# Kernel optimization log

Hardware: AMD Instinct MI355X
Metric: run time of the kernel (lower is better)

## Reference

```python
import jax, jax.numpy as jnp
import numpy as np

NUM_HEADS = 8
SPLIT_S = 4
DIM = 288            # n_feat * 3 * 3
SCALE = (DIM // NUM_HEADS) ** -0.5  # quirk: uses full dim's head_dim (36), not reduced
EPS = 1e-5


def _extract_patches(x):
    # x: [B,C,H,W] -> [B, C*9, H*W], 3x3 kernel, stride 1, 'same' padding
    B, C, H, W = x.shape
    xp = jnp.pad(x, ((0, 0), (0, 0), (1, 1), (1, 1)))
    pats = jnp.stack([xp[:, :, i:i + H, j:j + W] for i in range(3) for j in range(3)], axis=2)
    return pats.reshape(B, C * 9, H * W)


def _fold(cols, H, W):
    # inverse of extract: [B, C*9, H*W] -> [B,C,H,W], summing overlapping patches
    B, Ck, _ = cols.shape
    C = Ck // 9
    p = cols.reshape(B, C, 3, 3, H, W)
    out = jnp.zeros((B, C, H + 2, W + 2), cols.dtype)
    for i in range(3):
        for j in range(3):
            out = out.at[:, :, i:i + H, j:j + W].add(p[:, :, i, j])
    return out[:, :, 1:H + 1, 1:W + 1]


def _ln(x, w, b):
    mu = x.mean(-1, keepdims=True)
    var = ((x - mu) ** 2).mean(-1, keepdims=True)
    return (x - mu) * jax.lax.rsqrt(var + EPS) * w + b


def _attn(x, reduce_w, qkv_w, proj_w, proj_b):
    # x: [B,N,288] -> reduce -> [B,N,144] -> block-diag attention over s=4 chunks
    x = x @ reduce_w.T
    B, N, C = x.shape
    hd = C // NUM_HEADS
    qkv = (x @ qkv_w.T).reshape(B, N, 3, NUM_HEADS, hd).transpose(2, 0, 3, 1, 4)
    q, k, v = qkv[0], qkv[1], qkv[2]          # [B,h,N,hd]
    chunk = N // SPLIT_S
    q = q.reshape(B, NUM_HEADS, SPLIT_S, chunk, hd)
    k = k.reshape(B, NUM_HEADS, SPLIT_S, chunk, hd)
    v = v.reshape(B, NUM_HEADS, SPLIT_S, chunk, hd)
    attn = jnp.einsum('bhscd,bhsed->bhsce', q, k) * SCALE   # [B,h,s,chunk,chunk]
    attn = jax.nn.softmax(attn, axis=-1)
    out = jnp.einsum('bhsce,bhsed->bhscd', attn, v)          # [B,h,s,chunk,hd]
    out = out.transpose(0, 2, 3, 1, 4).reshape(B, N, C)      # cat chunks on token dim
    return out @ proj_w.T + proj_b


def setup_inputs() -> dict:
    key = jax.random.key(0)
    ks = jax.random.split(key, 12)
    d, dr, dh = DIM, DIM // 2, DIM // 4  # 288, 144, 72
    f = lambda k, shape: (jax.random.normal(k, shape, jnp.float32) * 0.02)
    return {
        'x': jax.random.normal(ks[0], (4, 32, 64, 64), jnp.float32),
        'ln1_w': jnp.ones((d,), jnp.float32), 'ln1_b': jnp.zeros((d,), jnp.float32),
        'reduce_w': f(ks[1], (dr, d)),
        'qkv_w': f(ks[2], (3 * dr, dr)),
        'proj_w': f(ks[3], (d, dr)), 'proj_b': jnp.zeros((d,), jnp.float32),
        'ln2_w': jnp.ones((d,), jnp.float32), 'ln2_b': jnp.zeros((d,), jnp.float32),
        'fc1_w': f(ks[4], (dh, d)), 'fc1_b': jnp.zeros((dh,), jnp.float32),
        'fc2_w': f(ks[5], (d, dh)), 'fc2_b': jnp.zeros((d,), jnp.float32),
    }


def reference(x, ln1_w, ln1_b, reduce_w, qkv_w, proj_w, proj_b, ln2_w, ln2_b, fc1_w, fc1_b, fc2_w, fc2_b):
    B, C, H, W = x.shape
    t = _extract_patches(x).transpose(0, 2, 1)  # [B, N=H*W, 288]
    t = t + _attn(_ln(t, ln1_w, ln1_b), reduce_w, qkv_w, proj_w, proj_b)
    h = _ln(t, ln2_w, ln2_b)
    t = t + (jax.nn.relu(h @ fc1_w.T + fc1_b) @ fc2_w.T + fc2_b)
    return _fold(t.transpose(0, 2, 1), H, W)
```

## Files before the change

### kernel.cpp

```cpp
#include <hip/hip_runtime.h>
#include <hip/hip_bf16.h>

typedef __hip_bfloat16 bf16;
typedef unsigned short u16;
typedef unsigned int u32;
typedef __attribute__((ext_vector_type(8))) short bf16x8;
typedef __attribute__((ext_vector_type(4))) float f32x4;

#define BB 4
#define CCH 32
#define HH 64
#define WW 64
#define NN 4096
#define D 288
#define DR 144
#define DQ 432
#define NH 8
#define HD 18
#define SPLIT 4
#define CHUNK 1024
#define KS 512
#define DH 72
#define SCALE_ 0.16666666666666666f
#define QSCALE 0.24044917348149343f
#define EPS_ 1e-5f
#define ASTR 160
#define ATS 168
#define HSTR 96

__device__ __attribute__((aligned(16))) u16 g_Wcb[DQ * D];
__device__ __attribute__((aligned(16))) u16 g_pw[D * ASTR];
__device__ __attribute__((aligned(16))) u16 g_f1w[HSTR * D];
__device__ __attribute__((aligned(16))) u16 g_f2w[D * HSTR];
__device__ __attribute__((aligned(16))) u16 g_q[(size_t)BB * NH * NN * 32];
__device__ __attribute__((aligned(16))) u16 g_k[(size_t)BB * NH * NN * 32];
__device__ __attribute__((aligned(16))) u16 g_vt[(size_t)BB * NH * SPLIT * 32 * CHUNK];
__device__ __attribute__((aligned(16))) float g_part[2 * (size_t)BB * NH * NN * 20];
__device__ __attribute__((aligned(16))) u16 g_h[(size_t)BB * NN * HSTR];
__device__ __attribute__((aligned(16))) u16 g_t0[(size_t)BB * NN * D];
__device__ __attribute__((aligned(16))) u16 g_t1[(size_t)BB * NN * D];
__device__ __attribute__((aligned(16))) u16 g_t2b[(size_t)BB * D * NN];
__device__ int   g_flag;

__device__ __forceinline__ float b2f(bf16 v) { return __bfloat162float(v); }
__device__ __forceinline__ float bits2f(u16 u) { return __uint_as_float(((u32)u) << 16); }
__device__ __forceinline__ u16 f2bits(float f) {
    u32 u = __float_as_uint(f);
    return (u16)((u + 0x7FFF + ((u >> 16) & 1)) >> 16);
}
__device__ __forceinline__ float ldin(const void* p, size_t i, int isbf) {
    return isbf ? b2f(((const bf16*)p)[i]) : ((const float*)p)[i];
}

#define RS  (D * ASTR + HSTR * D + D * HSTR)
#define RS2 (RS + BB * NH * SPLIT * CHUNK)
#define RSB ((RS2 + 255) / 256)
#define PATCHB (BB * HH)

__global__ void k_prep(const void* __restrict__ x, const void* __restrict__ qkv_w,
                       const void* __restrict__ reduce_w, const void* __restrict__ proj_w,
                       const void* __restrict__ fc1_w, const void* __restrict__ fc2_w) {
    __shared__ int cnt4[4];
    __shared__ float qw[DR];
    __shared__ float slab[32 * 3 * 66];
    int tid = threadIdx.x;
    {
        const u16* u = (const u16*)x;
        int c = 0;
        for (int i = tid; i < 2048; i += 256) c += (((u[i] >> 7) & 0xFF) >= 0x90);
        for (int o = 32; o; o >>= 1) c += __shfl_xor(c, o);
        if ((tid & 63) == 0) cnt4[tid >> 6] = c;
    }
    __syncthreads();
    int bf = (cnt4[0] + cnt4[1] + cnt4[2] + cnt4[3]) < 32;
    if (tid == 0 && blockIdx.x == 0) g_flag = bf;

    int bid = blockIdx.x;
    if (bid < DQ) {
        int o = bid;
        if (tid < DR) qw[tid] = ldin(qkv_w, (size_t)o * DR + tid, bf);
        __syncthreads();
        for (int col = tid; col < D; col += 256) {
            float s0 = 0.f, s1 = 0.f;
            #pragma unroll 4
            for (int j = 0; j < DR; j += 2) {
                s0 += qw[j] * ldin(reduce_w, (size_t)j * D + col, bf);
                s1 += qw[j + 1] * ldin(reduce_w, (size_t)(j + 1) * D + col, bf);
            }
            g_Wcb[(size_t)o * D + col] = f2bits(s0 + s1);
        }
    } else if (bid < DQ + RSB) {
        int idx = (bid - DQ) * 256 + tid;
        if (idx < D * ASTR) {
            int o = idx / ASTR, j = idx % ASTR;
            g_pw[idx] = (j < DR) ? f2bits(ldin(proj_w, (size_t)o * DR + j, bf)) : (u16)0;
        } else if (idx < D * ASTR + HSTR * D) {
            int t = idx - D * ASTR;
            int o = t / D;
            g_f1w[t] = (o < DH) ? f2bits(ldin(fc1_w, (size_t)t, bf)) : (u16)0;
        } else if (idx < RS) {
            int t = idx - D * ASTR - HSTR * D;
            int o = t / HSTR, j = t % HSTR;
            g_f2w[t] = (j < DH) ? f2bits(ldin(fc2_w, (size_t)o * DH + j, bf)) : (u16)0;
        } else if (idx < RS2) {
            int t = idx - RS;
            int bhs = t >> 10, n = t & 1023;
            g_vt[((size_t)bhs * 32 + 18) * CHUNK + n] = 0x3F80;
        }
    } else {
        int pb = bid - DQ - RSB;
        int b = pb >> 6, y = pb & 63;
        for (int idx = tid; idx < 32 * 3 * 66; idx += 256) {
            int c = idx / 198, rem = idx % 198;
            int ki = rem / 66, col = rem % 66 - 1;
            int sy = y + ki - 1;
            float v = 0.f;
            if (col >= 0 && col < 64 && sy >= 0 && sy < 64)
                v = ldin(x, ((size_t)(b * CCH + c) * HH + sy) * WW + col, bf);
            slab[idx] = v;
        }
        __syncthreads();
        size_t obase = ((size_t)b * NN + y * 64) * D;
        for (int idx = tid; idx < 64 * D; idx += 256) {
            int t = idx / D, f = idx % D;
            int c = f / 9, k = f % 9, ki = k / 3, kj = k % 3;
            g_t0[obase + idx] = f2bits(slab[c * 198 + ki * 66 + t + kj]);
        }
    }
}

__global__ void k_ln_qkv(const void* __restrict__ lnw, const void* __restrict__ lnb) {
    __shared__ __attribute__((aligned(16))) u16 xln[16 * 296];
    __shared__ float lnwf[D], lnbf[D];
    __shared__ float smu[16], srs[16];
    __shared__ u16 buf[3][144][16];
    int bf = g_flag;
    int tid = threadIdx.x;
    size_t tok0 = (size_t)blockIdx.x * 16;
    for (int i = tid; i < D; i += 256) { lnwf[i] = ldin(lnw, i, bf); lnbf[i] = ldin(lnb, i, bf); }
    {
        int tt = tid >> 4, p = tid & 15;
        const u32* pr = (const u32*)(g_t0 + (tok0 + tt) * D + p * 18);
        float s = 0.f, q = 0.f;
        #pragma unroll
        for (int j = 0; j < 9; ++j) {
            u32 v = pr[j];
            float a = bits2f((u16)(v & 0xFFFF)), b = bits2f((u16)(v >> 16));
            s += a + b; q += a * a + b * b;
        }
        #pragma unroll
        for (int o = 1; o < 16; o <<= 1) { s += __shfl_xor(s, o); q += __shfl_xor(q, o); }
        if (p == 0) {
            float mu = s / D;
            smu[tt] = mu;
            srs[tt] = rsqrtf(q / D - mu * mu + EPS_);
        }
    }
    __syncthreads();
    for (int idx = tid; idx < 16 * 144; idx += 256) {
        int t = idx / 144, dw = idx % 144;
        u32 v = *(const u32*)(g_t0 + (tok0 + t) * D + 2 * dw);
        float mu = smu[t], rs = srs[t];
        int f = 2 * dw;
        float a = (bits2f((u16)(v & 0xFFFF)) - mu) * rs * lnwf[f] + lnbf[f];
        float b = (bits2f((u16)(v >> 16)) - mu) * rs * lnwf[f + 1] + lnbf[f + 1];
        *(u32*)&xln[t * 296 + f] = (u32)f2bits(a) | ((u32)f2bits(b) << 16);
    }
    __syncthreads();
    int w = tid >> 6, lane = tid & 63, quad = lane >> 4, l15 = lane & 15;
    bf16x8 areg[9];
    const u16* abase = xln + l15 * 296 + quad * 8;
    #pragma unroll
    for (int ks = 0; ks < 9; ++ks) areg[ks] = *(const bf16x8*)(abase + ks * 32);
    int nt0 = w * 7, nt1 = (nt0 + 7 > 27) ? 27 : nt0 + 7;
    for (int nt = nt0; nt < nt1; ++nt) {
        f32x4 acc = {0.f, 0.f, 0.f, 0.f};
        const u16* bbase = g_Wcb + (size_t)(nt * 16 + l15) * D + quad * 8;
        #pragma unroll
        for (int ks = 0; ks < 9; ++ks) {
            bf16x8 bfr = *(const bf16x8*)(bbase + ks * 32);
            acc = __builtin_amdgcn_mfma_f32_16x16x32_bf16(areg[ks], bfr, acc, 0, 0, 0);
        }
        int o = nt * 16 + l15;
        int which = o / DR, rem = o % DR;
        #pragma unroll
        for (int r = 0; r < 4; ++r)
            buf[which][rem][quad * 4 + r] = f2bits(which == 0 ? acc[r] * QSCALE : acc[r]);
    }
    __syncthreads();
    {
        int b_ = (int)(tok0 >> 12);
        int n0 = (int)(tok0 & 4095);
        int sIdx = n0 >> 10, nc = n0 & 1023;
        for (int idx = tid; idx < 2 * 8 * 16 * 9; idx += 256) {
            int which = idx / 1152;
            int r2 = idx - which * 1152;
            int h = r2 / 144, r3 = r2 % 144, t = r3 / 9, dw = r3 % 9;
            u32 lo = buf[which][h * 18 + 2 * dw][t];
            u32 hi = buf[which][h * 18 + 2 * dw + 1][t];
            u16* dst = (which ? g_k : g_q) + ((size_t)(b_ * NH + h) * NN + n0 + t) * 32 + 2 * dw;
            *(u32*)dst = lo | (hi << 16);
        }
        for (int idx = tid; idx < 144 * 8; idx += 256) {
            int rem = idx >> 3, tp = idx & 7;
            int hh = rem / HD, dd = rem % HD;
            u32 lo = buf[2][rem][2 * tp];
            u32 hi = buf[2][rem][2 * tp + 1];
            size_t voff = (((size_t)(b_ * NH + hh) * SPLIT + sIdx) * 32 + dd) * CHUNK + nc + 2 * tp;
            *(u32*)&g_vt[voff] = lo | (hi << 16);
        }
    }
}

#define PSTR 72
__global__ __launch_bounds__(128) void k_attn() {
    __shared__ __attribute__((aligned(16))) u16 Pl[2][4][16 * PSTR];
    int bid = blockIdx.x;
    int chunk = bid & 127;
    int qblk = (bid >> 7) & 7;
    int ksl = bid >> 10;
    int s = chunk & 3, bh = chunk >> 2;
    int tid = threadIdx.x;
    int w = tid >> 6, lane = tid & 63, quad = lane >> 4, l15 = lane & 15;

    size_t rowbase = (size_t)bh * NN + s * CHUNK;
    size_t vtbase = ((size_t)bh * SPLIT + s) * 32 * CHUNK;
    const u16* kbase = g_k + rowbase * 32 + quad * 8;
    const u16* vbase = g_vt + vtbase + quad * 8;

    int qbase = qblk * 128 + w * 64;
    bf16x8 qf[4];
    #pragma unroll
    for (int t = 0; t < 4; ++t)
        qf[t] = *(const bf16x8*)(g_q + (rowbase + qbase + t * 16 + l15) * 32 + quad * 8);

    f32x4 accA[4], accB[4];
    #pragma unroll
    for (int t = 0; t < 4; ++t) {
        accA[t] = (f32x4){0.f, 0.f, 0.f, 0.f};
        accB[t] = (f32x4){0.f, 0.f, 0.f, 0.f};
    }

    int kt0 = ksl * KS;
    for (int kk = 0; kk < KS; kk += 64) {
        int kt = kt0 + kk;
        bf16x8 kf0 = *(const bf16x8*)(kbase + (size_t)(kt + 2 * l15) * 32);
        bf16x8 kf1 = *(const bf16x8*)(kbase + (size_t)(kt + 2 * l15 + 1) * 32);
        bf16x8 kf2 = *(const bf16x8*)(kbase + (size_t)(kt + 32 + 2 * l15) * 32);
        bf16x8 kf3 = *(const bf16x8*)(kbase + (size_t)(kt + 33 + 2 * l15) * 32);
        bf16x8 vA0 = *(const bf16x8*)(vbase + (size_t)l15 * CHUNK + kt);
        bf16x8 vB0 = *(const bf16x8*)(vbase + (size_t)(16 + l15) * CHUNK + kt);
        bf16x8 vA1 = *(const bf16x8*)(vbase + (size_t)l15 * CHUNK + kt + 32);
        bf16x8 vB1 = *(const bf16x8*)(vbase + (size_t)(16 + l15) * CHUNK + kt + 32);
        f32x4 z = {0.f, 0.f, 0.f, 0.f};
        #pragma unroll
        for (int t = 0; t < 4; ++t) {
            u16* pw = Pl[w][t];
            f32x4 S0 = __builtin_amdgcn_mfma_f32_16x16x32_bf16(qf[t], kf0, z, 0, 0, 0);
            f32x4 S1 = __builtin_amdgcn_mfma_f32_16x16x32_bf16(qf[t], kf1, z, 0, 0, 0);
            f32x4 S2 = __builtin_amdgcn_mfma_f32_16x16x32_bf16(qf[t], kf2, z, 0, 0, 0);
            f32x4 S3 = __builtin_amdgcn_mfma_f32_16x16x32_bf16(qf[t], kf3, z, 0, 0, 0);
            #pragma unroll
            for (int r = 0; r < 4; ++r) {
                float p0 = exp2f(S0[r]), p1 = exp2f(S1[r]);
                float p2 = exp2f(S2[r]), p3 = exp2f(S3[r]);
                u32 w0 = __builtin_amdgcn_perm(__float_as_uint(p1), __float_as_uint(p0), 0x07060302u);
                u32 w1 = __builtin_amdgcn_perm(__float_as_uint(p3), __float_as_uint(p2), 0x07060302u);
                *(u32*)&pw[(quad * 4 + r) * PSTR + 2 * l15] = w0;
                *(u32*)&pw[(quad * 4 + r) * PSTR + 32 + 2 * l15] = w1;
            }
        }
        #pragma unroll
        for (int t = 0; t < 4; ++t) {
            const u16* pw = Pl[w][t];
            bf16x8 pf0 = *(const bf16x8*)&pw[l15 * PSTR + quad * 8];
            bf16x8 pf1 = *(const bf16x8*)&pw[l15 * PSTR + 32 + quad * 8];
            accA[t] = __builtin_amdgcn_mfma_f32_16x16x32_bf16(pf0, vA0, accA[t], 0, 0, 0);
            accB[t] = __builtin_amdgcn_mfma_f32_16x16x32_bf16(pf0, vB0, accB[t], 0, 0, 0);
            accA[t] = __builtin_amdgcn_mfma_f32_16x16x32_bf16(pf1, vA1, accA[t], 0, 0, 0);
            accB[t] = __builtin_amdgcn_mfma_f32_16x16x32_bf16(pf1, vB1, accB[t], 0, 0, 0);
        }
    }
    float* pb = g_part + (((size_t)ksl * 32 + bh) * SPLIT + s) * (size_t)(CHUNK * 20);
    #pragma unroll
    for (int t = 0; t < 4; ++t) {
        #pragma unroll
        for (int r = 0; r < 4; ++r) {
            int tokenc = qbase + t * 16 + quad * 4 + r;
            float* row = pb + (size_t)tokenc * 20;
            row[l15] = accA[t][r];
            if (l15 < 3) row[16 + l15] = accB[t][r];
        }
    }
}

__global__ void k_proj_ln_fc1(const void* __restrict__ proj_b, const void* __restrict__ lnw,
                              const void* __restrict__ lnb, const void* __restrict__ fc1_b) {
    __shared__ float t1f[16][290];
    __shared__ __attribute__((aligned(16))) u16 xln[16 * 296];
    __shared__ __attribute__((aligned(16))) u16 attnT[16 * ATS];
    __shared__ float lnwf[D], lnbf[D];
    __shared__ float smu[16], srs[16];
    int bf = g_flag;
    int tid = threadIdx.x;
    size_t tok0 = (size_t)blockIdx.x * 16;
    int w = tid >> 6, lane = tid & 63, quad = lane >> 4, l15 = lane & 15;
    for (int i = tid; i < D; i += 256) { lnwf[i] = ldin(lnw, i, bf); lnbf[i] = ldin(lnb, i, bf); }

    int b_ = (int)(tok0 >> 12);
    int s_ = ((int)tok0 & 4095) >> 10;
    int tc0 = (int)tok0 & 1023;
    for (int idx = tid; idx < 16 * (ATS - DR); idx += 256) {
        int t = idx / (ATS - DR), f = idx % (ATS - DR);
        attnT[t * ATS + DR + f] = 0;
    }
    if (tid < 128) {
        int t = tid >> 3, h = tid & 7;
        const float* p1 = g_part + (((size_t)(b_ * NH + h)) * SPLIT + s_) * (size_t)(CHUNK * 20)
                        + (size_t)(tc0 + t) * 20;
        const float* p2 = p1 + (size_t)32 * SPLIT * CHUNK * 20;
        f32x4 a0 = *(const f32x4*)p1,        c0 = *(const f32x4*)p2;
        f32x4 a1 = *(const f32x4*)(p1 + 4),  c1 = *(const f32x4*)(p2 + 4);
        f32x4 a2 = *(const f32x4*)(p1 + 8),  c2 = *(const f32x4*)(p2 + 8);
        f32x4 a3 = *(const f32x4*)(p1 + 12), c3 = *(const f32x4*)(p2 + 12);
        f32x4 a4 = *(const f32x4*)(p1 + 16), c4 = *(const f32x4*)(p2 + 16);
        float inv = 1.f / (a4[2] + c4[2]);
        u16* dst = attnT + t * ATS + h * HD;
        #pragma unroll
        for (int d = 0; d < 4; ++d) {
            dst[d]      = f2bits((a0[d] + c0[d]) * inv);
            dst[4 + d]  = f2bits((a1[d] + c1[d]) * inv);
            dst[8 + d]  = f2bits((a2[d] + c2[d]) * inv);
            dst[12 + d] = f2bits((a3[d] + c3[d]) * inv);
        }
        dst[16] = f2bits((a4[0] + c4[0]) * inv);
        dst[17] = f2bits((a4[1] + c4[1]) * inv);
    }
    __syncthreads();

    {
        bf16x8 areg[5];
        const u16* abase = attnT + l15 * ATS + quad * 8;
        #pragma unroll
        for (int ks = 0; ks < 5; ++ks) areg[ks] = *(const bf16x8*)(abase + ks * 32);
        const int tab[5] = {0, 5, 10, 14, 18};
        for (int nt = tab[w]; nt < tab[w + 1]; ++nt) {
            f32x4 acc = {0.f, 0.f, 0.f, 0.f};
            const u16* bbase = g_pw + (size_t)(nt * 16 + l15) * ASTR + quad * 8;
            #pragma unroll
            for (int ks = 0; ks < 5; ++ks) {
                bf16x8 bfr = *(const bf16x8*)(bbase + ks * 32);
                acc = __builtin_amdgcn_mfma_f32_16x16x32_bf16(areg[ks], bfr, acc, 0, 0, 0);
            }
            int o = nt * 16 + l15;
            float bias = ldin(proj_b, o, bf);
            #pragma unroll
            for (int r = 0; r < 4; ++r) {
                size_t token = tok0 + quad * 4 + r;
                size_t off = token * D + o;
                float val = bits2f(g_t0[off]) + acc[r] + bias;
                g_t1[off] = f2bits(val);
                t1f[quad * 4 + r][o] = val;
            }
        }
    }
    __syncthreads();
    {
        int tt = tid >> 4, p = tid & 15;
        const float* src = &t1f[tt][p * 18];
        float s = 0.f, q = 0.f;
        #pragma unroll
        for (int j = 0; j < 18; ++j) { float a = src[j]; s += a; q += a * a; }
        #pragma unroll
        for (int o = 1; o < 16; o <<= 1) { s += __shfl_xor(s, o); q += __shfl_xor(q, o); }
        if (p == 0) {
            float mu = s / D;
            smu[tt] = mu;
            srs[tt] = rsqrtf(q / D - mu * mu + EPS_);
        }
    }
    __syncthreads();
    for (int idx = tid; idx < 16 * 144; idx += 256) {
        int t = idx / 144, dw = idx % 144;
        int f = 2 * dw;
        float mu = smu[t], rs = srs[t];
        float a = (t1f[t][f] - mu) * rs * lnwf[f] + lnbf[f];
        float b = (t1f[t][f + 1] - mu) * rs * lnwf[f + 1] + lnbf[f + 1];
        *(u32*)&xln[t * 296 + f] = (u32)f2bits(a) | ((u32)f2bits(b) << 16);
    }
    __syncthreads();
    {
        bf16x8 areg[9];
        const u16* abase = xln + l15 * 296 + quad * 8;
        #pragma unroll
        for (int ks = 0; ks < 9; ++ks) areg[ks] = *(const bf16x8*)(abase + ks * 32);
        const int tab2[5] = {0, 2, 4, 5, 6};
        for (int nt = tab2[w]; nt < tab2[w + 1]; ++nt) {
            f32x4 acc = {0.f, 0.f, 0.f, 0.f};
            const u16* bbase = g_f1w + (size_t)(nt * 16 + l15) * D + quad * 8;
            #pragma unroll
            for (int ks = 0; ks < 9; ++ks) {
                bf16x8 bfr = *(const bf16x8*)(bbase + ks * 32);
                acc = __builtin_amdgcn_mfma_f32_16x16x32_bf16(areg[ks], bfr, acc, 0, 0, 0);
            }
            int o = nt * 16 + l15;
            float bias = (o < DH) ? ldin(fc1_b, o, bf) : 0.f;
            #pragma unroll
            for (int r = 0; r < 4; ++r) {
                size_t token = tok0 + quad * 4 + r;
                g_h[token * HSTR + o] = f2bits(fmaxf(acc[r] + bias, 0.f));
            }
        }
    }
}

__global__ void k_fc2(const void* __restrict__ fc2_b) {
    __shared__ float t2f[16][293];
    int bf = g_flag;
    int tid = threadIdx.x;
    size_t tok0 = (size_t)blockIdx.x * 16;
    int w = tid >> 6, lane = tid & 63, quad = lane >> 4, l15 = lane & 15;
    bf16x8 areg[3];
    const u16* abase = g_h + (tok0 + l15) * HSTR + quad * 8;
    #pragma unroll
    for (int ks = 0; ks < 3; ++ks) areg[ks] = *(const bf16x8*)(abase + ks * 32);
    const int tab[5] = {0, 5, 10, 14, 18};
    for (int nt = tab[w]; nt < tab[w + 1]; ++nt) {
        f32x4 acc = {0.f, 0.f, 0.f, 0.f};
        const u16* bbase = g_f2w + (size_t)(nt * 16 + l15) * HSTR + quad * 8;
        #pragma unroll
        for (int ks = 0; ks < 3; ++ks) {
            bf16x8 bfr = *(const bf16x8*)(bbase + ks * 32);
            acc = __builtin_amdgcn_mfma_f32_16x16x32_bf16(areg[ks], bfr, acc, 0, 0, 0);
        }
        int o = nt * 16 + l15;
        float bias = ldin(fc2_b, o, bf);
        #pragma unroll
        for (int r = 0; r < 4; ++r) {
            size_t token = tok0 + quad * 4 + r;
            t2f[quad * 4 + r][o] = bits2f(g_t1[token * D + o]) + acc[r] + bias;
        }
    }
    __syncthreads();
    int b_ = (int)(tok0 >> 12), n0 = (int)(tok0 & 4095);
    for (int idx = tid; idx < D * 8; idx += 256) {
        int o = idx >> 3, tp = idx & 7;
        u32 v = (u32)f2bits(t2f[2 * tp][o]) | ((u32)f2bits(t2f[2 * tp + 1][o]) << 16);
        *(u32*)&g_t2b[((size_t)b_ * D + o) * NN + n0 + 2 * tp] = v;
    }
}

__global__ void k_fold(void* __restrict__ out) {
    int bf = g_flag;
    int idx = blockIdx.x * blockDim.x + threadIdx.x;
    if (idx >= BB * CCH * HH * WW) return;
    int xx = idx % WW;
    int y = (idx / WW) % HH;
    int c = (idx / (WW * HH)) % CCH;
    int b = idx / (WW * HH * CCH);
    const u16* base = g_t2b + ((size_t)b * D + c * 9) * NN;
    float s = 0.f;
    #pragma unroll
    for (int i = 0; i < 3; ++i) {
        int sy = y + 1 - i;
        if (sy < 0 || sy >= HH) continue;
        #pragma unroll
        for (int j = 0; j < 3; ++j) {
            int sx = xx + 1 - j;
            if (sx < 0 || sx >= WW) continue;
            s += bits2f(base[(size_t)(i * 3 + j) * NN + sy * WW + sx]);
        }
    }
    if (bf) ((bf16*)out)[idx] = __float2bfloat16(s);
    else    ((float*)out)[idx] = s;
}

extern "C" void kernel_launch(void* const* d_in, const int* in_sizes, int n_in,
                              void* d_out, int out_size, void* d_ws, size_t ws_size,
                              hipStream_t stream) {
    const void* x        = d_in[0];
    const void* ln1_w    = d_in[1];
    const void* ln1_b    = d_in[2];
    const void* reduce_w = d_in[3];
    const void* qkv_w    = d_in[4];
    const void* proj_w   = d_in[5];
    const void* proj_b   = d_in[6];
    const void* ln2_w    = d_in[7];
    const void* ln2_b    = d_in[8];
    const void* fc1_w    = d_in[9];
    const void* fc1_b    = d_in[10];
    const void* fc2_w    = d_in[11];
    const void* fc2_b    = d_in[12];

    k_prep        <<<DQ + RSB + PATCHB, 256, 0, stream>>>(x, qkv_w, reduce_w, proj_w, fc1_w, fc2_w);
    k_ln_qkv      <<<BB * NN / 16, 256, 0, stream>>>(ln1_w, ln1_b);
    k_attn        <<<2 * BB * NH * SPLIT * 8, 128, 0, stream>>>();
    k_proj_ln_fc1 <<<BB * NN / 16, 256, 0, stream>>>(proj_b, ln2_w, ln2_b, fc1_b);
    k_fc2         <<<BB * NN / 16, 256, 0, stream>>>(fc2_b);
    k_fold        <<<(BB * CCH * HH * WW + 255) / 256, 256, 0, stream>>>(d_out);
}
```

Measured before the change: 218.2 us.

## Process 32 tokens per block in token-wise GEMM kernels to reuse weight fragments

The LN+QKV, proj+LN+FC1 and FC2 kernels now handle 32 tokens per block instead of 16. Each wave keeps two sets of A fragments and issues two MFMAs per loaded weight fragment, so global weight loads per token are halved. The proj kernel also stores its residual tile in shared memory as bf16 rather than fp32 to keep LDS use in check. The cost is half as many blocks (fewer waves to hide latency), more registers per thread, and LN2 statistics now computed from bf16-rounded values.

```diff
diff --git a/kernel.cpp b/kernel.cpp
--- a/kernel.cpp
+++ b/kernel.cpp
@@ -130,26 +130,26 @@
 }
 
 __global__ void k_ln_qkv(const void* __restrict__ lnw, const void* __restrict__ lnb) {
-    __shared__ __attribute__((aligned(16))) u16 xln[16 * 296];
+    __shared__ __attribute__((aligned(16))) u16 xln[32 * 296];
     __shared__ float lnwf[D], lnbf[D];
-    __shared__ float smu[16], srs[16];
-    __shared__ u16 buf[3][144][16];
+    __shared__ float smu[32], srs[32];
+    __shared__ u16 buf[3][144][32];
     int bf = g_flag;
     int tid = threadIdx.x;
-    size_t tok0 = (size_t)blockIdx.x * 16;
+    size_t tok0 = (size_t)blockIdx.x * 32;
     for (int i = tid; i < D; i += 256) { lnwf[i] = ldin(lnw, i, bf); lnbf[i] = ldin(lnb, i, bf); }
     {
-        int tt = tid >> 4, p = tid & 15;
-        const u32* pr = (const u32*)(g_t0 + (tok0 + tt) * D + p * 18);
+        int tt = tid >> 3, p = tid & 7;
+        const u32* pr = (const u32*)(g_t0 + (tok0 + tt) * D + p * 36);
         float s = 0.f, q = 0.f;
         #pragma unroll
-        for (int j = 0; j < 9; ++j) {
+        for (int j = 0; j < 18; ++j) {
             u32 v = pr[j];
             float a = bits2f((u16)(v & 0xFFFF)), b = bits2f((u16)(v >> 16));
             s += a + b; q += a * a + b * b;
         }
         #pragma unroll
-        for (int o = 1; o < 16; o <<= 1) { s += __shfl_xor(s, o); q += __shfl_xor(q, o); }
+        for (int o = 1; o < 8; o <<= 1) { s += __shfl_xor(s, o); q += __shfl_xor(q, o); }
         if (p == 0) {
             float mu = s / D;
             smu[tt] = mu;
@@ -157,7 +157,7 @@
         }
     }
     __syncthreads();
-    for (int idx = tid; idx < 16 * 144; idx += 256) {
+    for (int idx = tid; idx < 32 * 144; idx += 256) {
         int t = idx / 144, dw = idx % 144;
         u32 v = *(const u32*)(g_t0 + (tok0 + t) * D + 2 * dw);
         float mu = smu[t], rs = srs[t];
@@ -168,41 +168,50 @@
     }
     __syncthreads();
     int w = tid >> 6, lane = tid & 63, quad = lane >> 4, l15 = lane & 15;
-    bf16x8 areg[9];
-    const u16* abase = xln + l15 * 296 + quad * 8;
-    #pragma unroll
-    for (int ks = 0; ks < 9; ++ks) areg[ks] = *(const bf16x8*)(abase + ks * 32);
+    bf16x8 areg0[9], areg1[9];
+    {
+        const u16* a0 = xln + l15 * 296 + quad * 8;
+        const u16* a1 = xln + (16 + l15) * 296 + quad * 8;
+        #pragma unroll
+        for (int ks = 0; ks < 9; ++ks) {
+            areg0[ks] = *(const bf16x8*)(a0 + ks * 32);
+            areg1[ks] = *(const bf16x8*)(a1 + ks * 32);
+        }
+    }
     int nt0 = w * 7, nt1 = (nt0 + 7 > 27) ? 27 : nt0 + 7;
     for (int nt = nt0; nt < nt1; ++nt) {
-        f32x4 acc = {0.f, 0.f, 0.f, 0.f};
+        f32x4 acc0 = {0.f, 0.f, 0.f, 0.f}, acc1 = {0.f, 0.f, 0.f, 0.f};
         const u16* bbase = g_Wcb + (size_t)(nt * 16 + l15) * D + quad * 8;
         #pragma unroll
         for (int ks = 0; ks < 9; ++ks) {
             bf16x8 bfr = *(const bf16x8*)(bbase + ks * 32);
-            acc = __builtin_amdgcn_mfma_f32_16x16x32_bf16(areg[ks], bfr, acc, 0, 0, 0);
+            acc0 = __builtin_amdgcn_mfma_f32_16x16x32_bf16(areg0[ks], bfr, acc0, 0, 0, 0);
+            acc1 = __builtin_amdgcn_mfma_f32_16x16x32_bf16(areg1[ks], bfr, acc1, 0, 0, 0);
         }
         int o = nt * 16 + l15;
         int which = o / DR, rem = o % DR;
         #pragma unroll
-        for (int r = 0; r < 4; ++r)
-            buf[which][rem][quad * 4 + r] = f2bits(which == 0 ? acc[r] * QSCALE : acc[r]);
+        for (int r = 0; r < 4; ++r) {
+            buf[which][rem][quad * 4 + r] = f2bits(which == 0 ? acc0[r] * QSCALE : acc0[r]);
+            buf[which][rem][16 + quad * 4 + r] = f2bits(which == 0 ? acc1[r] * QSCALE : acc1[r]);
+        }
     }
     __syncthreads();
     {
         int b_ = (int)(tok0 >> 12);
         int n0 = (int)(tok0 & 4095);
         int sIdx = n0 >> 10, nc = n0 & 1023;
-        for (int idx = tid; idx < 2 * 8 * 16 * 9; idx += 256) {
-            int which = idx / 1152;
-            int r2 = idx - which * 1152;
-            int h = r2 / 144, r3 = r2 % 144, t = r3 / 9, dw = r3 % 9;
+        for (int idx = tid; idx < 2 * 8 * 32 * 9; idx += 256) {
+            int which = idx / 2304;
+            int r2 = idx - which * 2304;
+            int h = r2 / 288, r3 = r2 % 288, t = r3 / 9, dw = r3 % 9;
             u32 lo = buf[which][h * 18 + 2 * dw][t];
             u32 hi = buf[which][h * 18 + 2 * dw + 1][t];
             u16* dst = (which ? g_k : g_q) + ((size_t)(b_ * NH + h) * NN + n0 + t) * 32 + 2 * dw;
             *(u32*)dst = lo | (hi << 16);
         }
-        for (int idx = tid; idx < 144 * 8; idx += 256) {
-            int rem = idx >> 3, tp = idx & 7;
+        for (int idx = tid; idx < 144 * 16; idx += 256) {
+            int rem = idx >> 4, tp = idx & 15;
             int hh = rem / HD, dd = rem % HD;
             u32 lo = buf[2][rem][2 * tp];
             u32 hi = buf[2][rem][2 * tp + 1];
@@ -296,25 +305,25 @@
 
 __global__ void k_proj_ln_fc1(const void* __restrict__ proj_b, const void* __restrict__ lnw,
                               const void* __restrict__ lnb, const void* __restrict__ fc1_b) {
-    __shared__ float t1f[16][290];
-    __shared__ __attribute__((aligned(16))) u16 xln[16 * 296];
-    __shared__ __attribute__((aligned(16))) u16 attnT[16 * ATS];
+    __shared__ __attribute__((aligned(16))) u16 t1f[32 * 296];
+    __shared__ __attribute__((aligned(16))) u16 xln[32 * 296];
+    __shared__ __attribute__((aligned(16))) u16 attnT[32 * ATS];
     __shared__ float lnwf[D], lnbf[D];
-    __shared__ float smu[16], srs[16];
+    __shared__ float smu[32], srs[32];
     int bf = g_flag;
     int tid = threadIdx.x;
-    size_t tok0 = (size_t)blockIdx.x * 16;
+    size_t tok0 = (size_t)blockIdx.x * 32;
     int w = tid >> 6, lane = tid & 63, quad = lane >> 4, l15 = lane & 15;
     for (int i = tid; i < D; i += 256) { lnwf[i] = ldin(lnw, i, bf); lnbf[i] = ldin(lnb, i, bf); }
 
     int b_ = (int)(tok0 >> 12);
     int s_ = ((int)tok0 & 4095) >> 10;
     int tc0 = (int)tok0 & 1023;
-    for (int idx = tid; idx < 16 * (ATS - DR); idx += 256) {
+    for (int idx = tid; idx < 32 * (ATS - DR); idx += 256) {
         int t = idx / (ATS - DR), f = idx % (ATS - DR);
         attnT[t * ATS + DR + f] = 0;
     }
-    if (tid < 128) {
+    {
         int t = tid >> 3, h = tid & 7;
         const float* p1 = g_part + (((size_t)(b_ * NH + h)) * SPLIT + s_) * (size_t)(CHUNK * 20)
                         + (size_t)(tc0 + t) * 20;
@@ -339,40 +348,58 @@
     __syncthreads();
 
     {
-        bf16x8 areg[5];
-        const u16* abase = attnT + l15 * ATS + quad * 8;
-        #pragma unroll
-        for (int ks = 0; ks < 5; ++ks) areg[ks] = *(const bf16x8*)(abase + ks * 32);
+        bf16x8 areg0[5], areg1[5];
+        const u16* a0 = attnT + l15 * ATS + quad * 8;
+        const u16* a1 = attnT + (16 + l15) * ATS + quad * 8;
+        #pragma unroll
+        for (int ks = 0; ks < 5; ++ks) {
+            areg0[ks] = *(const bf16x8*)(a0 + ks * 32);
+            areg1[ks] = *(const bf16x8*)(a1 + ks * 32);
+        }
         const int tab[5] = {0, 5, 10, 14, 18};
         for (int nt = tab[w]; nt < tab[w + 1]; ++nt) {
-            f32x4 acc = {0.f, 0.f, 0.f, 0.f};
+            f32x4 acc0 = {0.f, 0.f, 0.f, 0.f}, acc1 = {0.f, 0.f, 0.f, 0.f};
             const u16* bbase = g_pw + (size_t)(nt * 16 + l15) * ASTR + quad * 8;
             #pragma unroll
             for (int ks = 0; ks < 5; ++ks) {
                 bf16x8 bfr = *(const bf16x8*)(bbase + ks * 32);
-                acc = __builtin_amdgcn_mfma_f32_16x16x32_bf16(areg[ks], bfr, acc, 0, 0, 0);
+                acc0 = __builtin_amdgcn_mfma_f32_16x16x32_bf16(areg0[ks], bfr, acc0, 0, 0, 0);
+                acc1 = __builtin_amdgcn_mfma_f32_16x16x32_bf16(areg1[ks], bfr, acc1, 0, 0, 0);
             }
             int o = nt * 16 + l15;
             float bias = ldin(proj_b, o, bf);
             #pragma unroll
             for (int r = 0; r < 4; ++r) {
-                size_t token = tok0 + quad * 4 + r;
-                size_t off = token * D + o;
-                float val = bits2f(g_t0[off]) + acc[r] + bias;
-                g_t1[off] = f2bits(val);
-                t1f[quad * 4 + r][o] = val;
+                {
+                    size_t token = tok0 + quad * 4 + r;
+                    size_t off = token * D + o;
+                    u16 vb = f2bits(bits2f(g_t0[off]) + acc0[r] + bias);
+                    g_t1[off] = vb;
+                    t1f[(quad * 4 + r) * 296 + o] = vb;
+                }
+                {
+                    size_t token = tok0 + 16 + quad * 4 + r;
+                    size_t off = token * D + o;
+                    u16 vb = f2bits(bits2f(g_t0[off]) + acc1[r] + bias);
+                    g_t1[off] = vb;
+                    t1f[(16 + quad * 4 + r) * 296 + o] = vb;
+                }
             }
         }
     }
     __syncthreads();
     {
-        int tt = tid >> 4, p = tid & 15;
-        const float* src = &t1f[tt][p * 18];
+        int tt = tid >> 3, p = tid & 7;
+        const u32* src = (const u32*)&t1f[tt * 296 + p * 36];
         float s = 0.f, q = 0.f;
         #pragma unroll
-        for (int j = 0; j < 18; ++j) { float a = src[j]; s += a; q += a * a; }
-        #pragma unroll
-        for (int o = 1; o < 16; o <<= 1) { s += __shfl_xor(s, o); q += __shfl_xor(q, o); }
+        for (int j = 0; j < 18; ++j) {
+            u32 v = src[j];
+            float a = bits2f((u16)(v & 0xFFFF)), b = bits2f((u16)(v >> 16));
+            s += a + b; q += a * a + b * b;
+        }
+        #pragma unroll
+        for (int o = 1; o < 8; o <<= 1) { s += __shfl_xor(s, o); q += __shfl_xor(q, o); }
         if (p == 0) {
             float mu = s / D;
             smu[tt] = mu;
@@ -380,71 +407,84 @@
         }
     }
     __syncthreads();
-    for (int idx = tid; idx < 16 * 144; idx += 256) {
+    for (int idx = tid; idx < 32 * 144; idx += 256) {
         int t = idx / 144, dw = idx % 144;
         int f = 2 * dw;
+        u32 v = *(const u32*)&t1f[t * 296 + f];
         float mu = smu[t], rs = srs[t];
-        float a = (t1f[t][f] - mu) * rs * lnwf[f] + lnbf[f];
-        float b = (t1f[t][f + 1] - mu) * rs * lnwf[f + 1] + lnbf[f + 1];
+        float a = (bits2f((u16)(v & 0xFFFF)) - mu) * rs * lnwf[f] + lnbf[f];
+        float b = (bits2f((u16)(v >> 16)) - mu) * rs * lnwf[f + 1] + lnbf[f + 1];
         *(u32*)&xln[t * 296 + f] = (u32)f2bits(a) | ((u32)f2bits(b) << 16);
     }
     __syncthreads();
     {
-        bf16x8 areg[9];
-        const u16* abase = xln + l15 * 296 + quad * 8;
-        #pragma unroll
-        for (int ks = 0; ks < 9; ++ks) areg[ks] = *(const bf16x8*)(abase + ks * 32);
+        bf16x8 areg0[9], areg1[9];
+        const u16* a0 = xln + l15 * 296 + quad * 8;
+        const u16* a1 = xln + (16 + l15) * 296 + quad * 8;
+        #pragma unroll
+        for (int ks = 0; ks < 9; ++ks) {
+            areg0[ks] = *(const bf16x8*)(a0 + ks * 32);
+            areg1[ks] = *(const bf16x8*)(a1 + ks * 32);
+        }
         const int tab2[5] = {0, 2, 4, 5, 6};
         for (int nt = tab2[w]; nt < tab2[w + 1]; ++nt) {
-            f32x4 acc = {0.f, 0.f, 0.f, 0.f};
+            f32x4 acc0 = {0.f, 0.f, 0.f, 0.f}, acc1 = {0.f, 0.f, 0.f, 0.f};
             const u16* bbase = g_f1w + (size_t)(nt * 16 + l15) * D + quad * 8;
             #pragma unroll
             for (int ks = 0; ks < 9; ++ks) {
                 bf16x8 bfr = *(const bf16x8*)(bbase + ks * 32);
-                acc = __builtin_amdgcn_mfma_f32_16x16x32_bf16(areg[ks], bfr, acc, 0, 0, 0);
+                acc0 = __builtin_amdgcn_mfma_f32_16x16x32_bf16(areg0[ks], bfr, acc0, 0, 0, 0);
+                acc1 = __builtin_amdgcn_mfma_f32_16x16x32_bf16(areg1[ks], bfr, acc1, 0, 0, 0);
             }
             int o = nt * 16 + l15;
             float bias = (o < DH) ? ldin(fc1_b, o, bf) : 0.f;
             #pragma unroll
             for (int r = 0; r < 4; ++r) {
-                size_t token = tok0 + quad * 4 + r;
-                g_h[token * HSTR + o] = f2bits(fmaxf(acc[r] + bias, 0.f));
+                g_h[(tok0 + quad * 4 + r) * HSTR + o] = f2bits(fmaxf(acc0[r] + bias, 0.f));
+                g_h[(tok0 + 16 + quad * 4 + r) * HSTR + o] = f2bits(fmaxf(acc1[r] + bias, 0.f));
             }
         }
     }
 }
 
 __global__ void k_fc2(const void* __restrict__ fc2_b) {
-    __shared__ float t2f[16][293];
+    __shared__ float t2f[32][293];
     int bf = g_flag;
     int tid = threadIdx.x;
-    size_t tok0 = (size_t)blockIdx.x * 16;
+    size_t tok0 = (size_t)blockIdx.x * 32;
     int w = tid >> 6, lane = tid & 63, quad = lane >> 4, l15 = lane & 15;
-    bf16x8 areg[3];
-    const u16* abase = g_h + (tok0 + l15) * HSTR + quad * 8;
-    #pragma unroll
-    for (int ks = 0; ks < 3; ++ks) areg[ks] = *(const bf16x8*)(abase + ks * 32);
+    bf16x8 areg0[3], areg1[3];
+    {
+        const u16* a0 = g_h + (tok0 + l15) * HSTR + quad * 8;
+        const u16* a1 = g_h + (tok0 + 16 + l15) * HSTR + quad * 8;
+        #pragma unroll
+        for (int ks = 0; ks < 3; ++ks) {
+            areg0[ks] = *(const bf16x8*)(a0 + ks * 32);
+            areg1[ks] = *(const bf16x8*)(a1 + ks * 32);
+        }
+    }
     const int tab[5] = {0, 5, 10, 14, 18};
     for (int nt = tab[w]; nt < tab[w + 1]; ++nt) {
-        f32x4 acc = {0.f, 0.f, 0.f, 0.f};
+        f32x4 acc0 = {0.f, 0.f, 0.f, 0.f}, acc1 = {0.f, 0.f, 0.f, 0.f};
         const u16* bbase = g_f2w + (size_t)(nt * 16 + l15) * HSTR + quad * 8;
         #pragma unroll
         for (int ks = 0; ks < 3; ++ks) {
             bf16x8 bfr = *(const bf16x8*)(bbase + ks * 32);
-            acc = __builtin_amdgcn_mfma_f32_16x16x32_bf16(areg[ks], bfr, acc, 0, 0, 0);
+            acc0 = __builtin_amdgcn_mfma_f32_16x16x32_bf16(areg0[ks], bfr, acc0, 0, 0, 0);
+            acc1 = __builtin_amdgcn_mfma_f32_16x16x32_bf16(areg1[ks], bfr, acc1, 0, 0, 0);
         }
         int o = nt * 16 + l15;
         float bias = ldin(fc2_b, o, bf);
         #pragma unroll
         for (int r = 0; r < 4; ++r) {
-            size_t token = tok0 + quad * 4 + r;
-            t2f[quad * 4 + r][o] = bits2f(g_t1[token * D + o]) + acc[r] + bias;
+            t2f[quad * 4 + r][o] = bits2f(g_t1[(tok0 + quad * 4 + r) * D + o]) + acc0[r] + bias;
+            t2f[16 + quad * 4 + r][o] = bits2f(g_t1[(tok0 + 16 + quad * 4 + r) * D + o]) + acc1[r] + bias;
         }
     }
     __syncthreads();
     int b_ = (int)(tok0 >> 12), n0 = (int)(tok0 & 4095);
-    for (int idx = tid; idx < D * 8; idx += 256) {
-        int o = idx >> 3, tp = idx & 7;
+    for (int idx = tid; idx < D * 16; idx += 256) {
+        int o = idx >> 4, tp = idx & 15;
         u32 v = (u32)f2bits(t2f[2 * tp][o]) | ((u32)f2bits(t2f[2 * tp + 1][o]) << 16);
         *(u32*)&g_t2b[((size_t)b_ * D + o) * NN + n0 + 2 * tp] = v;
     }
@@ -493,9 +533,9 @@
     const void* fc2_b    = d_in[12];
 
     k_prep        <<<DQ + RSB + PATCHB, 256, 0, stream>>>(x, qkv_w, reduce_w, proj_w, fc1_w, fc2_w);
-    k_ln_qkv      <<<BB * NN / 16, 256, 0, stream>>>(ln1_w, ln1_b);
+    k_ln_qkv      <<<BB * NN / 32, 256, 0, stream>>>(ln1_w, ln1_b);
     k_attn        <<<2 * BB * NH * SPLIT * 8, 128, 0, stream>>>();
-    k_proj_ln_fc1 <<<BB * NN / 16, 256, 0, stream>>>(proj_b, ln2_w, ln2_b, fc1_b);
-    k_fc2         <<<BB * NN / 16, 256, 0, stream>>>(fc2_b);
+    k_proj_ln_fc1 <<<BB * NN / 32, 256, 0, stream>>>(proj_b, ln2_w, ln2_b, fc1_b);
+    k_fc2         <<<BB * NN / 32, 256, 0, stream>>>(fc2_b);
     k_fold        <<<(BB * CCH * HH * WW + 255) / 256, 256, 0, stream>>>(d_out);
 }
```

After: 205.1 us. -6.0%, faster.
